# Kernel tuning notes

Measured on AMD Instinct MI355X. Metric: run time of the kernel, lower is better.

Reference implementation:

```python
import jax
import jax.numpy as jnp
import numpy as np

N_WIRES = 4          # hardcoded by QLayer encoder (rx on wires 0..3)
H = N_WIRES          # hidden_dim must equal n_qubits for the gating elementwise math
T, B, D, TAGS = 512, 2048, 8, 16  # original unbinds dim 0, so dim0 = time, dim1 = batch


def apply_rx(state, theta, wire):
    """Apply RX(theta) on `wire`. state: (B,2,2,2,2) complex64, theta: (B,)."""
    st = jnp.moveaxis(state, 1 + wire, -1)
    a, b = st[..., 0], st[..., 1]
    th = theta[:, None, None, None] * 0.5
    c = jnp.cos(th)
    s = -1j * jnp.sin(th)
    st = jnp.stack([c * a + s * b, s * a + c * b], axis=-1)
    return jnp.moveaxis(st, -1, 1 + wire)


def apply_cnot(state, ctrl, tgt):
    st = jnp.moveaxis(state, (1 + ctrl, 1 + tgt), (-2, -1))  # (...,2,2)
    st = st.at[..., 1, :].set(st[..., 1, ::-1])
    return jnp.moveaxis(st, (-2, -1), (1 + ctrl, 1 + tgt))


def qlayer(angles, thetas):
    """QuantumQLSTM.QLayer: RX data encoding, trainable RX, CNOT ring, PauliZ expvals.
    angles: (B, 4) data angles; thetas: (4,) trainable RX angles -> (B, 4) expvals."""
    bsz = angles.shape[0]
    state = jnp.zeros((bsz, 16), jnp.complex64).at[:, 0].set(1.0)
    state = state.reshape(bsz, 2, 2, 2, 2)
    for w in range(N_WIRES):
        state = apply_rx(state, angles[:, w], w)
    for w in range(N_WIRES):
        state = apply_rx(state, jnp.broadcast_to(thetas[w], (bsz,)), w)
    for w in range(N_WIRES):  # cnot(w, w+1), last wraps to 0
        state = apply_cnot(state, w, (w + 1) % N_WIRES)
    probs = state.real ** 2 + state.imag ** 2  # (B,2,2,2,2)
    exps = []
    for w in range(N_WIRES):
        sign = jnp.array([1.0, -1.0], jnp.float32).reshape(
            [1] + [2 if i == w else 1 for i in range(N_WIRES)])
        exps.append(jnp.sum(probs * sign, axis=(1, 2, 3, 4)))
    return jnp.stack(exps, axis=-1)  # (B, 4)


def lstm_forward(x, w_gates, b_gates, rx_theta):
    # Faithful to torch: inputs.unbind(dim=0) -> scan over axis 0; batch = x.shape[1].
    bsz = x.shape[1]
    h0 = jnp.zeros((bsz, H), x.dtype)
    c0 = jnp.zeros((bsz, H), x.dtype)

    def step(carry, xt):
        hx, cx = carry
        comb = jnp.concatenate([xt, hx], axis=-1)                    # (B, D+H)
        pre = jnp.einsum('bd,gkd->gbk', comb, w_gates) + b_gates[:, None, :]  # (4,B,4)
        f = jax.nn.sigmoid(qlayer(pre[0], rx_theta[0]))
        i = jax.nn.sigmoid(qlayer(pre[1], rx_theta[1]))
        g = jnp.tanh(qlayer(pre[2], rx_theta[2]))
        o = jax.nn.sigmoid(qlayer(pre[3], rx_theta[3]))
        cx = f * cx + i * g
        hx = o * jnp.tanh(cx)
        return (hx, cx), hx

    _, outs = jax.lax.scan(jax.checkpoint(step), (h0, c0), x)
    return outs  # (T, B, H)


def setup_inputs() -> dict:
    key = jax.random.key(0)
    ks = jax.random.split(key, 6)
    x = jax.random.normal(ks[0], (T, B, D), jnp.float32)
    w_gates = jax.random.normal(ks[1], (4, N_WIRES, D + H), jnp.float32) * 0.3
    b_gates = jnp.zeros((4, N_WIRES), jnp.float32)
    rx_theta = jax.random.uniform(ks[2], (4, N_WIRES), jnp.float32, 0.0, 2.0 * np.pi)
    w_tag = jax.random.normal(ks[3], (TAGS, H), jnp.float32) * 0.3
    b_tag = jnp.zeros((TAGS,), jnp.float32)
    return {"x": x, "w_gates": w_gates, "b_gates": b_gates,
            "rx_theta": rx_theta, "w_tag": w_tag, "b_tag": b_tag}


def reference(x, w_gates, b_gates, rx_theta, w_tag, b_tag):
    # encode(): SamplerQNN has input_params=[], so it cannot transform features;
    # features pass through to the QLSTM (see notes).
    outs = lstm_forward(x, w_gates, b_gates, rx_theta)   # (T, B, H)
    logits = outs @ w_tag.T + b_tag                      # (T, B, TAGS)
    return jax.nn.log_softmax(logits, axis=-1)
```

## Files before the change

kernel.cpp:

```cpp
#include <hip/hip_runtime.h>

#define TT   512
#define BB   2048
#define NTAG 16
#define CH   8
#define NCH  (TT / CH)
#define BBN  (BB * NTAG)

typedef float v2f __attribute__((ext_vector_type(2)));

#define DPP_XOR1  0xB1
#define DPP_XOR2  0x4E
#define DPP_XOR3  0x1B
#define DPP_ROR4  0x124
#define DPP_ROR8  0x128
#define DPP_ROR12 0x12C

template<int CTRL>
__device__ __forceinline__ float dppf(float v) {
    int r = __builtin_amdgcn_update_dpp(0, __builtin_bit_cast(int, v),
                                        CTRL, 0xF, 0xF, true);
    return __builtin_bit_cast(float, r);
}

__global__ __launch_bounds__(192, 1) void qlstm_fused(
    const float* __restrict__ x,
    const float* __restrict__ w_gates,
    const float* __restrict__ b_gates,
    const float* __restrict__ rx_theta,
    const float* __restrict__ w_tag,
    const float* __restrict__ b_tag,
    float* __restrict__ out)
{
    __shared__ float  accL[2][2][CH][64];
    __shared__ float  hrng[2][2][CH][64];
    __shared__ float4 xstg[2][2][64];

    const int tid = threadIdx.x;
    const int wv  = tid >> 6;
    const int l   = tid & 63;
    const int e   = l >> 4;
    const int g   = (l >> 2) & 3;
    const int k   = l & 3;

    const float IV  = 0.15915494309189535f;
    const float L2E = 1.44269504088896f;
    const float LN2 = 0.69314718056f;

    if (wv == 0) {
        const float* wrow = w_gates + (g * 4 + k) * 12;
        const float wh0 = wrow[8 + (k ^ 0)] * IV;
        const float wh1 = wrow[8 + (k ^ 1)] * IV;
        const float wh2 = wrow[8 + (k ^ 2)] * IV;
        const float wh3 = wrow[8 + (k ^ 3)] * IV;

        const bool gt = (g == 2);
        const float ab = gt ? 0.0f : 0.5f;
        const float d0 = gt ? 0.999904f  : 0.25f;
        const float d1 = gt ? -0.331065f : -0.0208333333f;
        const float d2 = gt ? 0.120472f  : 0.00208333333f;
        const float d3 = gt ? -0.027717f : -2.10813e-4f;

        const float u0 = 0.999160f,  u1 = -0.325289f, u2 = 0.112257f;
        const float u3 = -0.028766f, u4 = 0.0043665f, u5 = -0.00028186f;

        const bool k0 = (k == 0), k1 = (k == 1), k3 = (k == 3);
        const bool g0 = (g == 0), g2 = (g == 2), glo = (g < 2);

        float hA = 0.f, h1A = 0.f, h2A = 0.f, h3A = 0.f, cA = 0.f;
        float hB = 0.f, h1B = 0.f, h2B = 0.f, h3B = 0.f, cB = 0.f;

        __syncthreads();

        for (int cc = 0; cc < NCH; ++cc) {
            const int cur = cc & 1;
            const float* apA = &accL[0][cur][0][l];
            const float* apB = &accL[1][cur][0][l];
            float* hpA = &hrng[0][cur][0][l];
            float* hpB = &hrng[1][cur][0][l];

            float aA = apA[0];
            float aB = apB[0];

            #pragma unroll
            for (int i = 0; i < CH; ++i) {
                float nA = aA, nB = aB;
                if (i + 1 < CH) {
                    nA = apA[(i + 1) * 64];
                    nB = apB[(i + 1) * 64];
                }

                float angA = fmaf(hA, wh0, aA);
                float angB = fmaf(hB, wh0, aB);
                angA = fmaf(h1A, wh1, angA);
                angB = fmaf(h1B, wh1, angB);
                angA = fmaf(h2A, wh2, angA);
                angB = fmaf(h2B, wh2, angB);
                angA = fmaf(h3A, wh3, angA);
                angB = fmaf(h3B, wh3, angB);

                const float CA = __builtin_amdgcn_cosf(angA);
                const float CB = __builtin_amdgcn_cosf(angB);

                const float m1A = dppf<DPP_XOR1>(CA);
                const float m1B = dppf<DPP_XOR1>(CB);
                const float m2A = dppf<DPP_XOR2>(CA);
                const float m2B = dppf<DPP_XOR2>(CB);
                const float m3A = dppf<DPP_XOR3>(CA);
                const float m3B = dppf<DPP_XOR3>(CB);
                const float BpA = m2A * m3A;
                const float BpB = m2B * m3B;
                const float ppA = CA * m1A;
                const float ppB = CB * m1B;
                const float XA = k0 ? m1A : (k3 ? ppA : CA);
                const float XB = k0 ? m1B : (k3 ? ppB : CB);
                const float YA = k1 ? m1A : BpA;
                const float YB = k1 ? m1B : BpB;
                const float qA = XA * YA;
                const float qB = XB * YB;

                const float yA  = qA * qA;
                const float yB  = qB * qB;
                const float y2A = yA * yA;
                const float y2B = yB * yB;
                const float paA = fmaf(yA, d1, d0);
                const float paB = fmaf(yB, d1, d0);
                const float pbA = fmaf(yA, d3, d2);
                const float pbB = fmaf(yB, d3, d2);
                const float PA  = fmaf(y2A, pbA, paA);
                const float PB  = fmaf(y2B, pbB, paB);
                const float actA = fmaf(qA, PA, ab);
                const float actB = fmaf(qB, PB, ab);

                const float rAA = dppf<DPP_ROR12>(actA);
                const float rAB = dppf<DPP_ROR12>(actB);
                const float rBA = dppf<DPP_ROR8>(actA);
                const float rBB = dppf<DPP_ROR8>(actB);
                const float rCA = dppf<DPP_ROR4>(actA);
                const float rCB = dppf<DPP_ROR4>(actB);
                cA = fmaf(actA, cA, rAA * rBA);
                cB = fmaf(actB, cB, rAB * rBB);

                const float cyA  = cA * cA;
                const float cyB  = cB * cB;
                const float cy2A = cyA * cyA;
                const float cy2B = cyB * cyB;
                const float t1A = fmaf(cyA, u1, u0);
                const float t1B = fmaf(cyB, u1, u0);
                const float t2A = fmaf(cyA, u3, u2);
                const float t2B = fmaf(cyB, u3, u2);
                const float t3A = fmaf(cyA, u5, u4);
                const float t3B = fmaf(cyB, u5, u4);
                const float t4A = fmaf(cy2A, t3A, t2A);
                const float t4B = fmaf(cy2B, t3B, t2B);
                const float PcA = fmaf(cy2A, t4A, t1A);
                const float PcB = fmaf(cy2B, t4B, t1B);
                const float vocA = rCA * cA;
                const float vocB = rCB * cB;
                const float hrA = PcA * vocA;
                const float hrB = PcB * vocB;

                hpA[i * 64] = hrA;
                hpB[i * 64] = hrB;

                const float r4A  = dppf<DPP_ROR4>(hrA);
                const float r4B  = dppf<DPP_ROR4>(hrB);
                const float r8A  = dppf<DPP_ROR8>(hrA);
                const float r8B  = dppf<DPP_ROR8>(hrB);
                const float r12A = dppf<DPP_ROR12>(hrA);
                const float r12B = dppf<DPP_ROR12>(hrB);
                hA = glo ? (g0 ? hrA : r4A) : (g2 ? r8A : r12A);
                hB = glo ? (g0 ? hrB : r4B) : (g2 ? r8B : r12B);

                h1A = dppf<DPP_XOR1>(hA);
                h1B = dppf<DPP_XOR1>(hB);
                h2A = dppf<DPP_XOR2>(hA);
                h2B = dppf<DPP_XOR2>(hB);
                h3A = dppf<DPP_XOR3>(hA);
                h3B = dppf<DPP_XOR3>(hB);

                aA = nA; aB = nB;
            }
            __syncthreads();
        }
    } else {
        const int s  = wv - 1;
        const int b0 = blockIdx.x * 8 + s * 4;

        const float* wrow = w_gates + (g * 4 + k) * 12;
        const v2f wp0 = { wrow[0] * IV, wrow[1] * IV };
        const v2f wp1 = { wrow[2] * IV, wrow[3] * IV };
        const v2f wp2 = { wrow[4] * IV, wrow[5] * IV };
        const v2f wp3 = { wrow[6] * IV, wrow[7] * IV };
        const v2f bp  = { (b_gates[g * 4 + k] + rx_theta[g * 4 + k]) * IV, 0.0f };

        const int tag = g * 4 + k;
        const float wt0 = w_tag[tag * 4 + (k ^ 0)] * L2E;
        const float wt1 = w_tag[tag * 4 + (k ^ 1)] * L2E;
        const float wt2 = w_tag[tag * 4 + (k ^ 2)] * L2E;
        const float wt3 = w_tag[tag * 4 + (k ^ 3)] * L2E;
        const float bt  = b_tag[tag] * L2E;

        const int hsl = e * 16 + k;
        float* outp = out + (size_t)b0 * NTAG + l;

        const float* xlane = x + (size_t)(l >> 3) * (BB * 8)
                               + (size_t)b0 * 8 + (l & 7) * 4;
        const size_t CHOFF = (size_t)CH * BB * 8;

        float4 reg = *(const float4*)(xlane);
        xstg[s][0][l] = reg;
        reg = *(const float4*)(xlane + CHOFF);
        xstg[s][1][l] = reg;
        {
            float* ap = &accL[s][0][0][l];
            #pragma unroll
            for (int i = 0; i < CH; ++i) {
                const float4 xA = xstg[s][0][i * 8 + 2 * e];
                const float4 xB = xstg[s][0][i * 8 + 2 * e + 1];
                const v2f a01 = { xA.x, xA.y }, a23 = { xA.z, xA.w };
                const v2f a45 = { xB.x, xB.y }, a67 = { xB.z, xB.w };
                v2f acc = __builtin_elementwise_fma(a01, wp0, bp);
                acc = __builtin_elementwise_fma(a23, wp1, acc);
                acc = __builtin_elementwise_fma(a45, wp2, acc);
                acc = __builtin_elementwise_fma(a67, wp3, acc);
                ap[i * 64] = acc.x + acc.y;
            }
        }
        reg = *(const float4*)(xlane + 2 * CHOFF);
        __syncthreads();

        for (int cc = 0; cc < NCH; ++cc) {
            const int cur = cc & 1;

            if (cc + 2 < NCH) {
                xstg[s][cur][l] = reg;
                const int cn = (cc + 3 < NCH) ? cc + 3 : NCH - 1;
                reg = *(const float4*)(xlane + (size_t)cn * CHOFF);
            }

            if (cc + 1 < NCH) {
                float* ap = &accL[s][cur ^ 1][0][l];
                #pragma unroll
                for (int i = 0; i < CH; ++i) {
                    const float4 xA = xstg[s][cur ^ 1][i * 8 + 2 * e];
                    const float4 xB = xstg[s][cur ^ 1][i * 8 + 2 * e + 1];
                    const v2f a01 = { xA.x, xA.y }, a23 = { xA.z, xA.w };
                    const v2f a45 = { xB.x, xB.y }, a67 = { xB.z, xB.w };
                    v2f acc = __builtin_elementwise_fma(a01, wp0, bp);
                    acc = __builtin_elementwise_fma(a23, wp1, acc);
                    acc = __builtin_elementwise_fma(a45, wp2, acc);
                    acc = __builtin_elementwise_fma(a67, wp3, acc);
                    ap[i * 64] = acc.x + acc.y;
                }
            }

            if (cc > 0) {
                const float* hp = &hrng[s][cur ^ 1][0][hsl];
                #pragma unroll
                for (int i = 0; i < CH; ++i) {
                    const float hv = hp[i * 64];
                    const float q1 = dppf<DPP_XOR1>(hv);
                    const float q2 = dppf<DPP_XOR2>(hv);
                    const float q3 = dppf<DPP_XOR3>(hv);

                    const float lgq = fmaf(hv, wt0, fmaf(q1, wt1, fmaf(q2, wt2,
                                         fmaf(q3, wt3, bt))));
                    const float ex = __builtin_amdgcn_exp2f(lgq);
                    float sm = ex + dppf<DPP_XOR1>(ex);
                    sm = sm + dppf<DPP_XOR2>(sm);
                    sm = sm + dppf<DPP_ROR4>(sm);
                    sm = sm + dppf<DPP_ROR8>(sm);
                    const float l2s = __builtin_amdgcn_logf(sm);

                    *outp = (lgq - l2s) * LN2;
                    outp += BBN;
                }
            }
            __syncthreads();
        }

        {
            const float* hp = &hrng[s][1][0][hsl];
            #pragma unroll
            for (int i = 0; i < CH; ++i) {
                const float hv = hp[i * 64];
                const float q1 = dppf<DPP_XOR1>(hv);
                const float q2 = dppf<DPP_XOR2>(hv);
                const float q3 = dppf<DPP_XOR3>(hv);

                const float lgq = fmaf(hv, wt0, fmaf(q1, wt1, fmaf(q2, wt2,
                                     fmaf(q3, wt3, bt))));
                const float ex = __builtin_amdgcn_exp2f(lgq);
                float sm = ex + dppf<DPP_XOR1>(ex);
                sm = sm + dppf<DPP_XOR2>(sm);
                sm = sm + dppf<DPP_ROR4>(sm);
                sm = sm + dppf<DPP_ROR8>(sm);
                const float l2s = __builtin_amdgcn_logf(sm);

                *outp = (lgq - l2s) * LN2;
                outp += BBN;
            }
        }
    }
}

extern "C" void kernel_launch(void* const* d_in, const int* in_sizes, int n_in,
                              void* d_out, int out_size, void* d_ws, size_t ws_size,
                              hipStream_t stream) {
    const float* x        = (const float*)d_in[0];
    const float* w_gates  = (const float*)d_in[1];
    const float* b_gates  = (const float*)d_in[2];
    const float* rx_theta = (const float*)d_in[3];
    const float* w_tag    = (const float*)d_in[4];
    const float* b_tag    = (const float*)d_in[5];
    float* out = (float*)d_out;

    qlstm_fused<<<BB / 8, 192, 0, stream>>>(x, w_gates, b_gates, rx_theta,
                                            w_tag, b_tag, out);
}
```

Before: 170.0 us.

## Split recurrent chain across two waves and recompute gate routing via DPP

Before, one wavefront ran two interleaved batch sub-groups (A/B) of the serial LSTM recurrence. Now two wavefronts each handle one sub-group, and the block grows to 256 threads. Each lane also now rebuilds f/i/g/o locally from rotated DPP values, so the extra DPP re-broadcast of h across gate groups goes away and the dependent chain per step gets shorter. This trades the ILP from interleaving two chains in one wave for wave-level parallelism, at the cost of an extra wave per block and more select logic.

```diff
diff --git a/kernel.cpp b/kernel.cpp
--- a/kernel.cpp
+++ b/kernel.cpp
@@ -23,7 +23,7 @@
     return __builtin_bit_cast(float, r);
 }
 
-__global__ __launch_bounds__(192, 1) void qlstm_fused(
+__global__ __launch_bounds__(256, 1) void qlstm_fused(
     const float* __restrict__ x,
     const float* __restrict__ w_gates,
     const float* __restrict__ b_gates,
@@ -47,7 +47,9 @@
     const float L2E = 1.44269504088896f;
     const float LN2 = 0.69314718056f;
 
-    if (wv == 0) {
+    if (wv < 2) {
+        const int s = wv;
+
         const float* wrow = w_gates + (g * 4 + k) * 12;
         const float wh0 = wrow[8 + (k ^ 0)] * IV;
         const float wh1 = wrow[8 + (k ^ 1)] * IV;
@@ -67,124 +69,76 @@
         const bool k0 = (k == 0), k1 = (k == 1), k3 = (k == 3);
         const bool g0 = (g == 0), g2 = (g == 2), glo = (g < 2);
 
-        float hA = 0.f, h1A = 0.f, h2A = 0.f, h3A = 0.f, cA = 0.f;
-        float hB = 0.f, h1B = 0.f, h2B = 0.f, h3B = 0.f, cB = 0.f;
+        float h = 0.f, h1 = 0.f, h2 = 0.f, h3 = 0.f, c = 0.f;
 
         __syncthreads();
 
         for (int cc = 0; cc < NCH; ++cc) {
             const int cur = cc & 1;
-            const float* apA = &accL[0][cur][0][l];
-            const float* apB = &accL[1][cur][0][l];
-            float* hpA = &hrng[0][cur][0][l];
-            float* hpB = &hrng[1][cur][0][l];
-
-            float aA = apA[0];
-            float aB = apB[0];
+
+            const float* ap = &accL[s][cur][0][l];
+            float a[CH];
+            #pragma unroll
+            for (int i = 0; i < CH; ++i) a[i] = ap[i * 64];
+
+            float* hp = &hrng[s][cur][0][l];
 
             #pragma unroll
             for (int i = 0; i < CH; ++i) {
-                float nA = aA, nB = aB;
-                if (i + 1 < CH) {
-                    nA = apA[(i + 1) * 64];
-                    nB = apB[(i + 1) * 64];
-                }
-
-                float angA = fmaf(hA, wh0, aA);
-                float angB = fmaf(hB, wh0, aB);
-                angA = fmaf(h1A, wh1, angA);
-                angB = fmaf(h1B, wh1, angB);
-                angA = fmaf(h2A, wh2, angA);
-                angB = fmaf(h2B, wh2, angB);
-                angA = fmaf(h3A, wh3, angA);
-                angB = fmaf(h3B, wh3, angB);
-
-                const float CA = __builtin_amdgcn_cosf(angA);
-                const float CB = __builtin_amdgcn_cosf(angB);
-
-                const float m1A = dppf<DPP_XOR1>(CA);
-                const float m1B = dppf<DPP_XOR1>(CB);
-                const float m2A = dppf<DPP_XOR2>(CA);
-                const float m2B = dppf<DPP_XOR2>(CB);
-                const float m3A = dppf<DPP_XOR3>(CA);
-                const float m3B = dppf<DPP_XOR3>(CB);
-                const float BpA = m2A * m3A;
-                const float BpB = m2B * m3B;
-                const float ppA = CA * m1A;
-                const float ppB = CB * m1B;
-                const float XA = k0 ? m1A : (k3 ? ppA : CA);
-                const float XB = k0 ? m1B : (k3 ? ppB : CB);
-                const float YA = k1 ? m1A : BpA;
-                const float YB = k1 ? m1B : BpB;
-                const float qA = XA * YA;
-                const float qB = XB * YB;
-
-                const float yA  = qA * qA;
-                const float yB  = qB * qB;
-                const float y2A = yA * yA;
-                const float y2B = yB * yB;
-                const float paA = fmaf(yA, d1, d0);
-                const float paB = fmaf(yB, d1, d0);
-                const float pbA = fmaf(yA, d3, d2);
-                const float pbB = fmaf(yB, d3, d2);
-                const float PA  = fmaf(y2A, pbA, paA);
-                const float PB  = fmaf(y2B, pbB, paB);
-                const float actA = fmaf(qA, PA, ab);
-                const float actB = fmaf(qB, PB, ab);
-
-                const float rAA = dppf<DPP_ROR12>(actA);
-                const float rAB = dppf<DPP_ROR12>(actB);
-                const float rBA = dppf<DPP_ROR8>(actA);
-                const float rBB = dppf<DPP_ROR8>(actB);
-                const float rCA = dppf<DPP_ROR4>(actA);
-                const float rCB = dppf<DPP_ROR4>(actB);
-                cA = fmaf(actA, cA, rAA * rBA);
-                cB = fmaf(actB, cB, rAB * rBB);
-
-                const float cyA  = cA * cA;
-                const float cyB  = cB * cB;
-                const float cy2A = cyA * cyA;
-                const float cy2B = cyB * cyB;
-                const float t1A = fmaf(cyA, u1, u0);
-                const float t1B = fmaf(cyB, u1, u0);
-                const float t2A = fmaf(cyA, u3, u2);
-                const float t2B = fmaf(cyB, u3, u2);
-                const float t3A = fmaf(cyA, u5, u4);
-                const float t3B = fmaf(cyB, u5, u4);
-                const float t4A = fmaf(cy2A, t3A, t2A);
-                const float t4B = fmaf(cy2B, t3B, t2B);
-                const float PcA = fmaf(cy2A, t4A, t1A);
-                const float PcB = fmaf(cy2B, t4B, t1B);
-                const float vocA = rCA * cA;
-                const float vocB = rCB * cB;
-                const float hrA = PcA * vocA;
-                const float hrB = PcB * vocB;
-
-                hpA[i * 64] = hrA;
-                hpB[i * 64] = hrB;
-
-                const float r4A  = dppf<DPP_ROR4>(hrA);
-                const float r4B  = dppf<DPP_ROR4>(hrB);
-                const float r8A  = dppf<DPP_ROR8>(hrA);
-                const float r8B  = dppf<DPP_ROR8>(hrB);
-                const float r12A = dppf<DPP_ROR12>(hrA);
-                const float r12B = dppf<DPP_ROR12>(hrB);
-                hA = glo ? (g0 ? hrA : r4A) : (g2 ? r8A : r12A);
-                hB = glo ? (g0 ? hrB : r4B) : (g2 ? r8B : r12B);
-
-                h1A = dppf<DPP_XOR1>(hA);
-                h1B = dppf<DPP_XOR1>(hB);
-                h2A = dppf<DPP_XOR2>(hA);
-                h2B = dppf<DPP_XOR2>(hB);
-                h3A = dppf<DPP_XOR3>(hA);
-                h3B = dppf<DPP_XOR3>(hB);
-
-                aA = nA; aB = nB;
+                float ang = fmaf(h,  wh0, a[i]);
+                ang = fmaf(h1, wh1, ang);
+                ang = fmaf(h2, wh2, ang);
+                ang = fmaf(h3, wh3, ang);
+
+                const float C = __builtin_amdgcn_cosf(ang);
+                const float m1 = dppf<DPP_XOR1>(C);
+                const float m2 = dppf<DPP_XOR2>(C);
+                const float m3 = dppf<DPP_XOR3>(C);
+                const float Bp  = m2 * m3;
+                const float pp  = C * m1;
+                const float F1  = k0 ? m1 : C;
+                const float F1b = k3 ? pp : F1;
+                const float F2  = k1 ? m1 : Bp;
+                const float q   = F1b * F2;
+
+                const float y  = q * q;
+                const float y2 = y * y;
+                const float tA = fmaf(y, d1, d0);
+                const float tB = fmaf(y, d3, d2);
+                const float P  = fmaf(y2, tB, tA);
+                const float act = fmaf(q, P, ab);
+
+                const float rA = dppf<DPP_ROR12>(act);
+                const float rB = dppf<DPP_ROR8>(act);
+                const float rC = dppf<DPP_ROR4>(act);
+                const float f_ = glo ? (g0 ? act : rC) : (g2 ? rB : rA);
+                const float i_ = glo ? (g0 ? rA : act) : (g2 ? rC : rB);
+                const float gg = glo ? (g0 ? rB : rA) : (g2 ? act : rC);
+                const float o_ = glo ? (g0 ? rC : rB) : (g2 ? rA : act);
+
+                c = fmaf(f_, c, i_ * gg);
+
+                const float cy  = c * c;
+                const float cy2 = cy * cy;
+                const float t1  = fmaf(cy, u1, u0);
+                const float t2  = fmaf(cy, u3, u2);
+                const float t3  = fmaf(cy, u5, u4);
+                const float t4  = fmaf(cy2, t3, t2);
+                const float Pc  = fmaf(cy2, t4, t1);
+                const float voc = o_ * c;
+                const float hr  = Pc * voc;
+
+                hp[i * 64] = hr;
+
+                h  = hr;
+                h1 = dppf<DPP_XOR1>(hr);
+                h2 = dppf<DPP_XOR2>(hr);
+                h3 = dppf<DPP_XOR3>(hr);
             }
             __syncthreads();
         }
     } else {
-        const int s  = wv - 1;
+        const int s  = wv - 2;
         const int b0 = blockIdx.x * 8 + s * 4;
 
         const float* wrow = w_gates + (g * 4 + k) * 12;
@@ -316,6 +270,6 @@
     const float* b_tag    = (const float*)d_in[5];
     float* out = (float*)d_out;
 
-    qlstm_fused<<<BB / 8, 192, 0, stream>>>(x, w_gates, b_gates, rx_theta,
+    qlstm_fused<<<BB / 8, 256, 0, stream>>>(x, w_gates, b_gates, rx_theta,
                                             w_tag, b_tag, out);
 }
```

After: 145.4 us. 1.17x faster.
